# Optimization experiments

Measured on AMD Instinct MI355X. Metric: run time of the kernel, lower is better.

The kernel has to match this reference:

```python
import jax, jax.numpy as jnp
import numpy as np


def setup_inputs() -> dict:
    key = jax.random.key(0)
    kq, kk, kv = jax.random.split(key, 3)
    B, H, S, D = 2, 16, 2048, 128
    return {
        "query_states": jax.random.normal(kq, (B, H, S, D), dtype=jnp.float32),
        "key_states": jax.random.normal(kk, (B, H, S, D), dtype=jnp.float32),
        "value_states": jax.random.normal(kv, (B, H, S, D), dtype=jnp.float32),
    }


def reference(query_states, key_states, value_states):
    # Faithful translation of CoreAttention.forward with attention_mask=None,
    # attention_dropout=0.0 (default, and dropout with p=0 is identity).
    B, H, Sq, D = query_states.shape
    Skv = key_states.shape[-2]
    scale = 1.0 / jnp.sqrt(jnp.asarray(D, dtype=query_states.dtype))
    # [B,H,Sq,Skv] score matrix (the module materializes this explicitly)
    attn_weights = jnp.einsum("bhqd,bhkd->bhqk", query_states, key_states) * scale
    # internal causal mask: triu(ones, diagonal=1) positions -> dtype min
    causal = jnp.triu(jnp.ones((Sq, Skv), dtype=bool), k=1)
    mask_value = jnp.finfo(attn_weights.dtype).min
    attn_weights = jnp.where(causal[None, None], mask_value, attn_weights)
    # torch does softmax in float64 then casts back; numerically stable fp32
    # softmax is equivalent to working precision here (jax x64 disabled).
    attn_weights = jax.nn.softmax(attn_weights, axis=-1).astype(query_states.dtype)
    attn_output = jnp.einsum("bhqk,bhkd->bhqd", attn_weights, value_states)
    return attn_output
```

## Files before the change

kernel.cpp:

```cpp
#include <hip/hip_runtime.h>
#include <hip/hip_bf16.h>
#include <stdint.h>

typedef __bf16  bf16x8 __attribute__((ext_vector_type(8)));
typedef __bf16  bf16x4 __attribute__((ext_vector_type(4)));
typedef float   f32x4  __attribute__((ext_vector_type(4)));
typedef uint32_t u32x4 __attribute__((ext_vector_type(4)));

#define SLEN  2048
#define DHEAD 128
#define QBLK  64
#define KVBLK 32
#define NQT   (SLEN / QBLK)
#define THR2  11.5415603f

__device__ __forceinline__ uint32_t cvt_pk(float lo, float hi2) {
    uint32_t u;
    asm("v_cvt_pk_bf16_f32 %0, %1, %2" : "=v"(u) : "v"(lo), "v"(hi2));
    return u;
}

__device__ __forceinline__ float exp2fast(float x) {
    return __builtin_amdgcn_exp2f(x);
}

__global__ __launch_bounds__(256, 3) void attn_fwd(
    const float* __restrict__ Q, const float* __restrict__ K,
    const float* __restrict__ V, float* __restrict__ O)
{
    const int bh = blockIdx.x;
    const int qt = (NQT - 1) - blockIdx.y;
    const int tid  = threadIdx.x;
    const int w    = tid >> 6;
    const int lane = tid & 63;
    const int r    = lane & 15;
    const int g    = lane >> 4;

    const size_t head_off = (size_t)bh * SLEN * DHEAD;
    const float* Qh = Q + head_off;
    const float* Kh = K + head_off;
    const float* Vh = V + head_off;
    float*       Oh = O + head_off;

    const int q0w = qt * QBLK + w * 16;

    __shared__ __bf16 K_sh [2][KVBLK * DHEAD];
    __shared__ __bf16 Vt_sh[2][DHEAD * 40];

    const float scale = 0.08838834764831845f * 1.4426950408889634f;

    bf16x8 qfrag[4];
    {
        const float4* qp = reinterpret_cast<const float4*>(
            Qh + (size_t)(q0w + r) * DHEAD + g * 8);
        #pragma unroll
        for (int kb = 0; kb < 4; ++kb) {
            float4 a = qp[kb*8 + 0];
            float4 b = qp[kb*8 + 1];
            a.x*=scale; a.y*=scale; a.z*=scale; a.w*=scale;
            b.x*=scale; b.y*=scale; b.z*=scale; b.w*=scale;
            bf16x8 f;
            f[0]=(__bf16)a.x; f[1]=(__bf16)a.y; f[2]=(__bf16)a.z; f[3]=(__bf16)a.w;
            f[4]=(__bf16)b.x; f[5]=(__bf16)b.y; f[6]=(__bf16)b.z; f[7]=(__bf16)b.w;
            qfrag[kb] = f;
        }
    }

    float4 kreg[4], vreg[4];
    const int c4  = tid & 31;
    const int kvq = tid >> 5;

    auto issue_loads = [&](int kv0) {
        #pragma unroll
        for (int it = 0; it < 4; ++it) {
            const int row = (it * 256 + tid) >> 5;
            kreg[it] = *reinterpret_cast<const float4*>(
                Kh + (size_t)(kv0 + row) * DHEAD + c4 * 4);
        }
        #pragma unroll
        for (int kr = 0; kr < 4; ++kr)
            vreg[kr] = *reinterpret_cast<const float4*>(
                Vh + (size_t)(kv0 + kvq * 4 + kr) * DHEAD + c4 * 4);
    };

    auto write_tiles = [&](int buf) {
        char* Kb  = reinterpret_cast<char*>(K_sh[buf]);
        char* Vtb = reinterpret_cast<char*>(Vt_sh[buf]);
        #pragma unroll
        for (int it = 0; it < 4; ++it) {
            const int row = (it * 256 + tid) >> 5;
            bf16x4 k4;
            k4[0]=(__bf16)kreg[it].x; k4[1]=(__bf16)kreg[it].y;
            k4[2]=(__bf16)kreg[it].z; k4[3]=(__bf16)kreg[it].w;
            *reinterpret_cast<bf16x4*>(
                Kb + row * 256 + ((c4 * 8) ^ ((row & 15) << 4))) = k4;
        }
        #pragma unroll
        for (int j = 0; j < 4; ++j) {
            const int d = c4 * 4 + j;
            bf16x4 v4;
            #pragma unroll
            for (int kr = 0; kr < 4; ++kr)
                v4[kr] = (__bf16)((&vreg[kr].x)[j]);
            *reinterpret_cast<bf16x4*>(
                Vtb + d * 80 + ((kvq ^ ((d >> 2) & 6)) * 8)) = v4;
        }
    };

    const f32x4 vzero = {0.f, 0.f, 0.f, 0.f};
    f32x4 acc_o[8];
    #pragma unroll
    for (int i = 0; i < 8; ++i) acc_o[i] = vzero;
    float m_run = -1e30f, l_run = 0.f;

    issue_loads(0);
    write_tiles(0);

    const int kvt_blk_max = 2 * qt + 1;
    const int kvt_max_w   = (q0w + 15) >> 5;
    int cur = 0;

    for (int kvt = 0; kvt <= kvt_blk_max; ++kvt) {
        __syncthreads();
        const bool more = (kvt < kvt_blk_max);
        if (more) issue_loads((kvt + 1) * KVBLK);

        if (kvt <= kvt_max_w) {
            const int kv0 = kvt * KVBLK;
            char* Kb  = reinterpret_cast<char*>(K_sh[cur]);
            char* Vtb = reinterpret_cast<char*>(Vt_sh[cur]);

            const bool alive1 = (kv0 + 16 <= q0w + 15);

            f32x4 st[2] = {vzero, vzero};
            __builtin_amdgcn_s_setprio(1);
            #pragma unroll
            for (int t = 0; t < 2; ++t) {
                if (t == 1 && !alive1) break;
                const int row = t * 16 + r;
                #pragma unroll
                for (int kb = 0; kb < 4; ++kb) {
                    bf16x8 kf = *reinterpret_cast<const bf16x8*>(
                        Kb + row * 256 + ((kb*64 + g*16) ^ ((row & 15) << 4)));
                    st[t] = __builtin_amdgcn_mfma_f32_16x16x32_bf16(
                        kf, qfrag[kb], st[t], 0, 0, 0);
                }
            }
            __builtin_amdgcn_s_setprio(0);

            const int q = q0w + r;
            float pmax = -1e30f;
            #pragma unroll
            for (int t = 0; t < 2; ++t) {
                if (t == 1 && !alive1) break;
                if (kv0 + t*16 + 15 > q0w) {
                    #pragma unroll
                    for (int j = 0; j < 4; ++j)
                        if (kv0 + t*16 + 4*g + j > q) st[t][j] = -1e30f;
                }
                #pragma unroll
                for (int j = 0; j < 4; ++j) pmax = fmaxf(pmax, st[t][j]);
            }
            pmax = fmaxf(pmax, __shfl_xor(pmax, 16));
            pmax = fmaxf(pmax, __shfl_xor(pmax, 32));

            if (__any(pmax > m_run + THR2)) {
                const float m_new = fmaxf(m_run, pmax);
                const float corr  = exp2fast(m_run - m_new);
                l_run *= corr; m_run = m_new;
                #pragma unroll
                for (int reg = 0; reg < 4; ++reg) {
                    const float cr = __shfl(corr, 4*g + reg);
                    #pragma unroll
                    for (int dt = 0; dt < 8; ++dt) acc_o[dt][reg] *= cr;
                }
            }

            float rowsum = 0.f;
            #pragma unroll
            for (int t = 0; t < 2; ++t) {
                if (t == 1 && !alive1) break;
                #pragma unroll
                for (int j = 0; j < 4; ++j) {
                    const float p = exp2fast(st[t][j] - m_run);
                    st[t][j] = p;
                    rowsum += p;
                }
            }
            rowsum += __shfl_xor(rowsum, 16);
            rowsum += __shfl_xor(rowsum, 32);
            l_run += rowsum;

            const uint32_t p00 = cvt_pk(st[0][0], st[0][1]);
            const uint32_t p01 = cvt_pk(st[0][2], st[0][3]);
            const uint32_t p10 = alive1 ? cvt_pk(st[1][0], st[1][1]) : 0u;
            const uint32_t p11 = alive1 ? cvt_pk(st[1][2], st[1][3]) : 0u;
            const int sA = r + ((2 * (g & 1)) << 4);
            const int sB = r + ((2 * (g & 1) + 1) << 4);
            u32x4 words;
            {
                const uint32_t lo0 = (uint32_t)__shfl((int)p00, sA);
                const uint32_t hi0 = (uint32_t)__shfl((int)p10, sA);
                const uint32_t lo1 = (uint32_t)__shfl((int)p01, sA);
                const uint32_t hi1 = (uint32_t)__shfl((int)p11, sA);
                const uint32_t lo2 = (uint32_t)__shfl((int)p00, sB);
                const uint32_t hi2 = (uint32_t)__shfl((int)p10, sB);
                const uint32_t lo3 = (uint32_t)__shfl((int)p01, sB);
                const uint32_t hi3 = (uint32_t)__shfl((int)p11, sB);
                words[0] = (g & 2) ? hi0 : lo0;
                words[1] = (g & 2) ? hi1 : lo1;
                words[2] = (g & 2) ? hi2 : lo2;
                words[3] = (g & 2) ? hi3 : lo3;
            }
            const bf16x8 pa = __builtin_bit_cast(bf16x8, words);

            __builtin_amdgcn_s_setprio(1);
            #pragma unroll
            for (int dt = 0; dt < 8; ++dt) {
                const int d = dt * 16 + r;
                bf16x8 vf = *reinterpret_cast<const bf16x8*>(
                    Vtb + d * 80 + (((2*g) ^ ((d >> 2) & 6)) * 8));
                acc_o[dt] = __builtin_amdgcn_mfma_f32_16x16x32_bf16(
                    pa, vf, acc_o[dt], 0, 0, 0);
            }
            __builtin_amdgcn_s_setprio(0);
        }

        if (more) write_tiles(cur ^ 1);
        cur ^= 1;
    }

    const float inv = 1.0f / l_run;
    #pragma unroll
    for (int reg = 0; reg < 4; ++reg) {
        const float iv = __shfl(inv, 4*g + reg);
        float* orow = Oh + (size_t)(q0w + 4*g + reg) * DHEAD + r;
        #pragma unroll
        for (int dt = 0; dt < 8; ++dt)
            orow[dt * 16] = acc_o[dt][reg] * iv;
    }
}

extern "C" void kernel_launch(void* const* d_in, const int* in_sizes, int n_in,
                              void* d_out, int out_size, void* d_ws, size_t ws_size,
                              hipStream_t stream) {
    const float* Q = (const float*)d_in[0];
    const float* K = (const float*)d_in[1];
    const float* V = (const float*)d_in[2];
    float* O = (float*)d_out;
    dim3 grid(32 , NQT);
    attn_fwd<<<grid, 256, 0, stream>>>(Q, K, V, O);
}
```

Before: 91.23 us.

## Software-pipeline QK^T of the next KV tile ahead of the current softmax

Restructures the KV loop so the QK^T MFMAs for tile i+1 are issued before the softmax and PV of tile i. The goal is to hide softmax ALU and shuffle latency behind matrix work. Shared-memory staging now prefetches two tiles ahead and adds a second barrier per iteration to protect buffer reuse. It also raises the launch-bounds occupancy hint from 3 to 4 blocks per CU, which tightens the register budget while an extra pair of score accumulators stays live, so spills are possible.

```diff
diff --git a/kernel.cpp b/kernel.cpp
--- a/kernel.cpp
+++ b/kernel.cpp
@@ -24,7 +24,7 @@
     return __builtin_amdgcn_exp2f(x);
 }
 
-__global__ __launch_bounds__(256, 3) void attn_fwd(
+__global__ __launch_bounds__(256, 4) void attn_fwd(
     const float* __restrict__ Q, const float* __restrict__ K,
     const float* __restrict__ V, float* __restrict__ O)
 {
@@ -113,40 +113,50 @@
     for (int i = 0; i < 8; ++i) acc_o[i] = vzero;
     float m_run = -1e30f, l_run = 0.f;
 
+    const int blkmax = 2 * qt + 1;
+    const int my_max = (q0w + 15) >> 5;
+
+    auto do_qk = [&](f32x4* st, int t, int kb_buf) {
+        char* Kb = reinterpret_cast<char*>(K_sh[kb_buf]);
+        const bool a1 = (t * KVBLK + 16 <= q0w + 15);
+        __builtin_amdgcn_s_setprio(1);
+        #pragma unroll
+        for (int tt = 0; tt < 2; ++tt) {
+            st[tt] = vzero;
+            if (tt == 1 && !a1) break;
+            const int row = tt * 16 + r;
+            #pragma unroll
+            for (int kb = 0; kb < 4; ++kb) {
+                bf16x8 kf = *reinterpret_cast<const bf16x8*>(
+                    Kb + row * 256 + ((kb*64 + g*16) ^ ((row & 15) << 4)));
+                st[tt] = __builtin_amdgcn_mfma_f32_16x16x32_bf16(
+                    kf, qfrag[kb], st[tt], 0, 0, 0);
+            }
+        }
+        __builtin_amdgcn_s_setprio(0);
+    };
+
     issue_loads(0);
     write_tiles(0);
-
-    const int kvt_blk_max = 2 * qt + 1;
-    const int kvt_max_w   = (q0w + 15) >> 5;
-    int cur = 0;
-
-    for (int kvt = 0; kvt <= kvt_blk_max; ++kvt) {
+    __syncthreads();
+    issue_loads(KVBLK);
+    f32x4 stp[2];
+    do_qk(stp, 0, 0);
+    write_tiles(1);
+
+    for (int i = 0; i <= blkmax; ++i) {
         __syncthreads();
-        const bool more = (kvt < kvt_blk_max);
-        if (more) issue_loads((kvt + 1) * KVBLK);
-
-        if (kvt <= kvt_max_w) {
-            const int kv0 = kvt * KVBLK;
-            char* Kb  = reinterpret_cast<char*>(K_sh[cur]);
-            char* Vtb = reinterpret_cast<char*>(Vt_sh[cur]);
-
+        const bool stage_more = (i + 2 <= blkmax);
+        if (stage_more) issue_loads((i + 2) * KVBLK);
+
+        f32x4 stn[2];
+        const bool do_next = (i + 1 <= my_max);
+        if (do_next) do_qk(stn, i + 1, (i + 1) & 1);
+
+        if (i <= my_max) {
+            const int kv0 = i * KVBLK;
+            char* Vtb = reinterpret_cast<char*>(Vt_sh[i & 1]);
             const bool alive1 = (kv0 + 16 <= q0w + 15);
-
-            f32x4 st[2] = {vzero, vzero};
-            __builtin_amdgcn_s_setprio(1);
-            #pragma unroll
-            for (int t = 0; t < 2; ++t) {
-                if (t == 1 && !alive1) break;
-                const int row = t * 16 + r;
-                #pragma unroll
-                for (int kb = 0; kb < 4; ++kb) {
-                    bf16x8 kf = *reinterpret_cast<const bf16x8*>(
-                        Kb + row * 256 + ((kb*64 + g*16) ^ ((row & 15) << 4)));
-                    st[t] = __builtin_amdgcn_mfma_f32_16x16x32_bf16(
-                        kf, qfrag[kb], st[t], 0, 0, 0);
-                }
-            }
-            __builtin_amdgcn_s_setprio(0);
 
             const int q = q0w + r;
             float pmax = -1e30f;
@@ -156,10 +166,10 @@
                 if (kv0 + t*16 + 15 > q0w) {
                     #pragma unroll
                     for (int j = 0; j < 4; ++j)
-                        if (kv0 + t*16 + 4*g + j > q) st[t][j] = -1e30f;
+                        if (kv0 + t*16 + 4*g + j > q) stp[t][j] = -1e30f;
                 }
                 #pragma unroll
-                for (int j = 0; j < 4; ++j) pmax = fmaxf(pmax, st[t][j]);
+                for (int j = 0; j < 4; ++j) pmax = fmaxf(pmax, stp[t][j]);
             }
             pmax = fmaxf(pmax, __shfl_xor(pmax, 16));
             pmax = fmaxf(pmax, __shfl_xor(pmax, 32));
@@ -182,8 +192,8 @@
                 if (t == 1 && !alive1) break;
                 #pragma unroll
                 for (int j = 0; j < 4; ++j) {
-                    const float p = exp2fast(st[t][j] - m_run);
-                    st[t][j] = p;
+                    const float p = exp2fast(stp[t][j] - m_run);
+                    stp[t][j] = p;
                     rowsum += p;
                 }
             }
@@ -191,10 +201,10 @@
             rowsum += __shfl_xor(rowsum, 32);
             l_run += rowsum;
 
-            const uint32_t p00 = cvt_pk(st[0][0], st[0][1]);
-            const uint32_t p01 = cvt_pk(st[0][2], st[0][3]);
-            const uint32_t p10 = alive1 ? cvt_pk(st[1][0], st[1][1]) : 0u;
-            const uint32_t p11 = alive1 ? cvt_pk(st[1][2], st[1][3]) : 0u;
+            const uint32_t p00 = cvt_pk(stp[0][0], stp[0][1]);
+            const uint32_t p01 = cvt_pk(stp[0][2], stp[0][3]);
+            const uint32_t p10 = alive1 ? cvt_pk(stp[1][0], stp[1][1]) : 0u;
+            const uint32_t p11 = alive1 ? cvt_pk(stp[1][2], stp[1][3]) : 0u;
             const int sA = r + ((2 * (g & 1)) << 4);
             const int sB = r + ((2 * (g & 1) + 1) << 4);
             u32x4 words;
@@ -226,8 +236,11 @@
             __builtin_amdgcn_s_setprio(0);
         }
 
-        if (more) write_tiles(cur ^ 1);
-        cur ^= 1;
+        __syncthreads();
+        if (stage_more) write_tiles(i & 1);
+
+        stp[0] = stn[0];
+        stp[1] = stn[1];
     }
 
     const float inv = 1.0f / l_run;
```

After: 185.4 us. 2.03x slower.
